# Performance work log

Hardware: AMD Instinct MI355X
Metric: run time of the kernel (lower is better)

The kernel has to match this reference:

```python
import jax, jax.numpy as jnp
import numpy as np

B, S, HID = 1, 2048, 4096
H, HKV, DFULL, D = 32, 8, 128, 96
GROUPS = H // HKV
SCALE = DFULL ** -0.5  # scaling uses the FULL head_dim per the source
ROPE_THETA = 10000.0


def setup_inputs() -> dict:
    key = jax.random.key(0)
    ks = jax.random.split(key, 8)
    hidden_states = jax.random.normal(ks[0], (B, S, HID), jnp.float32)
    # standard HF Llama RoPE tables over the FULL head dim
    inv_freq = 1.0 / (ROPE_THETA ** (jnp.arange(0, DFULL, 2, dtype=jnp.float32) / DFULL))
    ang = jnp.arange(S, dtype=jnp.float32)[:, None] * inv_freq[None, :]  # [S, DFULL/2]
    emb = jnp.concatenate([ang, ang], axis=-1)  # [S, DFULL]
    cos = jnp.cos(emb)[None]  # [1, S, DFULL]
    sin = jnp.sin(emb)[None]
    # per-kv-head frequency indices: lo half in [0, DFULL/2), hi half = lo + DFULL/2
    half, dh = DFULL // 2, D // 2
    idx_lo = jax.random.randint(ks[1], (HKV, dh), 0, half)
    indices = jnp.concatenate([idx_lo, idx_lo + half], axis=-1).astype(jnp.int32)  # [HKV, D]
    s = 0.02
    Wq = jax.random.normal(ks[2], (H * D, HID), jnp.float32) * s
    Wk = jax.random.normal(ks[3], (HKV * D, HID), jnp.float32) * s
    Wv = jax.random.normal(ks[4], (HKV * D, HID), jnp.float32) * s
    Wo = jax.random.normal(ks[5], (HID, H * D), jnp.float32) * s
    return {"hidden_states": hidden_states, "cos": cos, "sin": sin,
            "indices": indices, "Wq": Wq, "Wk": Wk, "Wv": Wv, "Wo": Wo}


def rotate_half(x):
    x1, x2 = jnp.split(x, 2, axis=-1)
    return jnp.concatenate([-x2, x1], axis=-1)


def reference(hidden_states, cos, sin, indices, Wq, Wk, Wv, Wo):
    b, s, _ = hidden_states.shape
    # QKV projections (no bias), reshape to [B, heads, S, D]
    q = (hidden_states @ Wq.T).reshape(b, s, H, D).transpose(0, 2, 1, 3)
    k = (hidden_states @ Wk.T).reshape(b, s, HKV, D).transpose(0, 2, 1, 3)
    v = (hidden_states @ Wv.T).reshape(b, s, HKV, D).transpose(0, 2, 1, 3)
    # indexed RoPE: gather per-kv-head frequencies from the full-dim tables
    cos_h = cos[:, :, indices].transpose(0, 2, 1, 3)  # [B, HKV, S, D]
    sin_h = sin[:, :, indices].transpose(0, 2, 1, 3)
    cos_q = jnp.repeat(cos_h, GROUPS, axis=1)  # [B, H, S, D]
    sin_q = jnp.repeat(sin_h, GROUPS, axis=1)
    q = q * cos_q + rotate_half(q) * sin_q
    k = k * cos_h + rotate_half(k) * sin_h
    # GQA: repeat kv to num_attention_heads
    k = jnp.repeat(k, GROUPS, axis=1)  # [B, H, S, D]
    v = jnp.repeat(v, GROUPS, axis=1)
    scores = jnp.einsum('bhqd,bhkd->bhqk', q, k) * SCALE
    causal = jnp.tril(jnp.ones((s, s), dtype=bool))
    scores = jnp.where(causal[None, None], scores, jnp.finfo(scores.dtype).min)
    probs = jax.nn.softmax(scores, axis=-1)
    out = jnp.einsum('bhqk,bhkd->bhqd', probs, v)  # [B, H, S, D]
    out = out.transpose(0, 2, 1, 3).reshape(b, s, H * D)
    return out @ Wo.T
```

## Files before the change

### kernel.cpp

```cpp
#include <hip/hip_runtime.h>

typedef unsigned short u16;
typedef unsigned int u32;
typedef __bf16 bf16x8 __attribute__((ext_vector_type(8)));
typedef float f32x4 __attribute__((ext_vector_type(4)));

#define SCALE_Q2 0.12751743443398106f

#define GLDS16(gp, lp)                                                        \
  __builtin_amdgcn_global_load_lds(                                           \
      (const __attribute__((address_space(1))) void*)(gp),                    \
      (__attribute__((address_space(3))) void*)(lp), 16, 0, 0)

__device__ __forceinline__ u16 f2bf(float f) {
  u32 u = __builtin_bit_cast(u32, f);
  u += 0x7fffu + ((u >> 16) & 1u);
  return (u16)(u >> 16);
}
__device__ __forceinline__ float bf2f(u16 b) {
  u32 u = ((u32)b) << 16;
  return __builtin_bit_cast(float, u);
}

__global__ __launch_bounds__(256) void cvt_kernel(const float* __restrict__ src,
                                                  u16* __restrict__ dst, int n4) {
  int i = blockIdx.x * 256 + threadIdx.x;
  if (i >= n4) return;
  float4 v = ((const float4*)src)[i];
  u32 lo = (u32)f2bf(v.x) | ((u32)f2bf(v.y) << 16);
  u32 hi = (u32)f2bf(v.z) | ((u32)f2bf(v.w) << 16);
  ((uint2*)dst)[i] = make_uint2(lo, hi);
}

template <bool BF16OUT>
__global__ __launch_bounds__(256) void gemm_bt(const u16* __restrict__ A,
                                               const u16* __restrict__ B,
                                               void* __restrict__ Cout,
                                               int M, int N, int K) {
  __shared__ u16 As[128 * 64];
  __shared__ u16 Bs[128 * 64];
  const int tid = threadIdx.x;
  const int w = tid >> 6, lane = tid & 63, quad = lane >> 4, c16 = lane & 15;
  const int m0 = blockIdx.y * 128, n0 = blockIdx.x * 128;
  const int wm = (w & 1) * 64, wn = (w >> 1) * 64;
  const int srow8 = lane >> 3;
  const int scg = (lane & 7) ^ srow8;

  f32x4 acc[4][4];
#pragma unroll
  for (int i = 0; i < 4; i++)
#pragma unroll
    for (int j = 0; j < 4; j++) acc[i][j] = (f32x4){0.f, 0.f, 0.f, 0.f};

  const u16* Abase = A + (size_t)(m0 + w * 8 + srow8) * K + scg * 8;
  const u16* Bbase = B + (size_t)(n0 + w * 8 + srow8) * K + scg * 8;

  for (int k0 = 0; k0 < K; k0 += 64) {
    __syncthreads();
#pragma unroll
    for (int it = 0; it < 4; it++) {
      GLDS16(Abase + (size_t)(it * 32) * K + k0, &As[(w * 8 + it * 32) * 64]);
      GLDS16(Bbase + (size_t)(it * 32) * K + k0, &Bs[(w * 8 + it * 32) * 64]);
    }
    __syncthreads();
#pragma unroll
    for (int kk = 0; kk < 2; kk++) {
      bf16x8 af[4], bf[4];
#pragma unroll
      for (int mt = 0; mt < 4; mt++) {
        int row = wm + mt * 16 + c16;
        int col = (kk * 4 + quad) ^ (row & 7);
        af[mt] = *(const bf16x8*)(&As[row * 64 + col * 8]);
      }
#pragma unroll
      for (int nt = 0; nt < 4; nt++) {
        int row = wn + nt * 16 + c16;
        int col = (kk * 4 + quad) ^ (row & 7);
        bf[nt] = *(const bf16x8*)(&Bs[row * 64 + col * 8]);
      }
#pragma unroll
      for (int mt = 0; mt < 4; mt++)
#pragma unroll
        for (int nt = 0; nt < 4; nt++)
          acc[mt][nt] = __builtin_amdgcn_mfma_f32_16x16x32_bf16(af[mt], bf[nt], acc[mt][nt], 0, 0, 0);
    }
  }
#pragma unroll
  for (int mt = 0; mt < 4; mt++)
#pragma unroll
    for (int nt = 0; nt < 4; nt++)
#pragma unroll
      for (int r = 0; r < 4; r++) {
        int m = m0 + wm + mt * 16 + quad * 4 + r;
        int n = n0 + wn + nt * 16 + c16;
        if (BF16OUT)
          ((u16*)Cout)[(size_t)m * N + n] = f2bf(acc[mt][nt][r]);
        else
          ((float*)Cout)[(size_t)m * N + n] = acc[mt][nt][r];
      }
}

__global__ __launch_bounds__(256) void rope_kernel(const u16* __restrict__ qkv,
                                                   const float* __restrict__ cosb,
                                                   const float* __restrict__ sinb,
                                                   const int* __restrict__ idxs,
                                                   u16* __restrict__ qB,
                                                   u16* __restrict__ kB) {
  u32 i = blockIdx.x * 256u + threadIdx.x;
  const u32 NQ = 2048u * 32u * 96u;
  if (i < NQ) {
    u32 s = i / 3072u, rem = i % 3072u;
    u32 h = rem / 96u, d = rem % 96u;
    u32 hkv = h >> 2;
    u32 base = s * 4608u + h * 96u + d;
    float x = bf2f(qkv[base]);
    float pv = (d < 48u) ? -bf2f(qkv[base + 48u]) : bf2f(qkv[base - 48u]);
    int idx = idxs[hkv * 96u + d];
    float c = cosb[s * 128u + idx], sn = sinb[s * 128u + idx];
    qB[(h * 2048u + s) * 96u + d] = f2bf((x * c + pv * sn) * SCALE_Q2);
  } else {
    u32 j = i - NQ;
    u32 s = j / 768u, rem = j % 768u;
    u32 hkv = rem / 96u, d = rem % 96u;
    u32 base = s * 4608u + 3072u + hkv * 96u + d;
    float x = bf2f(qkv[base]);
    float pv = (d < 48u) ? -bf2f(qkv[base + 48u]) : bf2f(qkv[base - 48u]);
    int idx = idxs[hkv * 96u + d];
    float c = cosb[s * 128u + idx], sn = sinb[s * 128u + idx];
    kB[(hkv * 2048u + s) * 96u + d] = f2bf(x * c + pv * sn);
  }
}

__global__ __launch_bounds__(256) void vtrans_kernel(const u16* __restrict__ qkvB,
                                                     u16* __restrict__ vtB) {
  __shared__ u16 T[64 * 34];
  const int s0 = blockIdx.x * 64, d0 = blockIdx.y * 32;
  const int tx = threadIdx.x & 31, ty = threadIdx.x >> 5;
#pragma unroll
  for (int it = 0; it < 8; it++) {
    int row = it * 8 + ty;
    T[row * 34 + tx] = qkvB[(size_t)(s0 + row) * 4608 + 3840 + d0 + tx];
  }
  __syncthreads();
  const int sx = threadIdx.x & 63, dy = threadIdx.x >> 6;
#pragma unroll
  for (int it = 0; it < 8; it++) {
    int d = it * 4 + dy;
    vtB[(size_t)(d0 + d) * 2048 + s0 + sx] = T[sx * 34 + d];
  }
}

__global__ __launch_bounds__(256) void attn_kernel(const u16* __restrict__ qB,
                                                   const u16* __restrict__ kB,
                                                   const u16* __restrict__ vtB,
                                                   u16* __restrict__ aoB) {
  __shared__ u16 Ks[64 * 96];
  __shared__ u16 Vs[96 * 64];
  __shared__ u16 Ps[4 * 16 * 64];
  const int tid = threadIdx.x;
  const int w = tid >> 6, lane = tid & 63, quad = lane >> 4, c16 = lane & 15;
  const int pr = blockIdx.x, h = blockIdx.y, hkv = h >> 2;
  u16* pw = Ps + w * (16 * 64);

  size_t voff[3];
#pragma unroll
  for (int it = 0; it < 3; it++) {
    int j = it * 256 + tid;
    int row = j >> 3, c = (j & 7) ^ (row & 7);
    voff[it] = (size_t)row * 2048 + c * 8;
  }
  const u16* kbase = kB + (size_t)hkv * 2048 * 96;
  const u16* vbase = vtB + (size_t)hkv * 96 * 2048;

  bf16x8 vones;
#pragma unroll
  for (int i = 0; i < 8; i++) vones[i] = (__bf16)1.0f;

  for (int ph = 0; ph < 2; ph++) {
    const int qt = ph ? (31 - pr) : pr;
    const int m_base = qt * 64 + w * 16;

    bf16x8 qf[3];
    {
      const u16* qrow = qB + ((size_t)h * 2048 + m_base + c16) * 96;
#pragma unroll
      for (int t = 0; t < 3; t++) qf[t] = *(const bf16x8*)(qrow + t * 32 + quad * 8);
    }
    f32x4 o[6], ol;
#pragma unroll
    for (int dt = 0; dt < 6; dt++) o[dt] = (f32x4){0.f, 0.f, 0.f, 0.f};
    ol = (f32x4){0.f, 0.f, 0.f, 0.f};

    for (int kt = 0; kt <= qt; kt++) {
      const int k0 = kt * 64;
      __syncthreads();
#pragma unroll
      for (int it = 0; it < 3; it++) {
        GLDS16(kbase + (size_t)k0 * 96 + (it * 256 + tid) * 8,
               &Ks[(it * 256 + w * 64) * 8]);
        GLDS16(vbase + voff[it] + k0, &Vs[(it * 256 + w * 64) * 8]);
      }
      __syncthreads();

      f32x4 sacc[4];
#pragma unroll
      for (int nt = 0; nt < 4; nt++) sacc[nt] = (f32x4){0.f, 0.f, 0.f, 0.f};
#pragma unroll
      for (int nt = 0; nt < 4; nt++)
#pragma unroll
        for (int t = 0; t < 3; t++) {
          bf16x8 kf = *(const bf16x8*)(&Ks[(nt * 16 + c16) * 96 + t * 32 + quad * 8]);
          sacc[nt] = __builtin_amdgcn_mfma_f32_16x16x32_bf16(qf[t], kf, sacc[nt], 0, 0, 0);
        }

      if (kt == qt) {
#pragma unroll
        for (int r = 0; r < 4; r++) {
          int row_abs = m_base + quad * 4 + r;
#pragma unroll
          for (int nt = 0; nt < 4; nt++)
            if (k0 + nt * 16 + c16 > row_abs) sacc[nt][r] = -__builtin_inff();
        }
      }

#pragma unroll
      for (int r = 0; r < 4; r++) {
        int mrow = quad * 4 + r, m7 = mrow & 7;
#pragma unroll
        for (int nt = 0; nt < 4; nt++) {
          float p = __builtin_amdgcn_exp2f(sacc[nt][r]);
          int chunk = (nt * 2 + (c16 >> 3)) ^ m7;
          pw[mrow * 64 + chunk * 8 + (c16 & 7)] =
              (u16)(__builtin_bit_cast(u32, p) >> 16);
        }
      }
      bf16x8 pf[2];
#pragma unroll
      for (int kti = 0; kti < 2; kti++) {
        int chunk = (kti * 4 + quad) ^ (c16 & 7);
        pf[kti] = *(const bf16x8*)(&pw[c16 * 64 + chunk * 8]);
      }
#pragma unroll
      for (int kti = 0; kti < 2; kti++) {
        ol = __builtin_amdgcn_mfma_f32_16x16x32_bf16(pf[kti], vones, ol, 0, 0, 0);
#pragma unroll
        for (int dt = 0; dt < 6; dt++) {
          int row = dt * 16 + c16;
          int vch = (kti * 4 + quad) ^ (row & 7);
          bf16x8 vf = *(const bf16x8*)(&Vs[row * 64 + vch * 8]);
          o[dt] = __builtin_amdgcn_mfma_f32_16x16x32_bf16(pf[kti], vf, o[dt], 0, 0, 0);
        }
      }
    }

#pragma unroll
    for (int r = 0; r < 4; r++) {
      float inv = 1.0f / ol[r];
      int row = m_base + quad * 4 + r;
#pragma unroll
      for (int dt = 0; dt < 6; dt++)
        aoB[(size_t)row * 3072 + h * 96 + dt * 16 + c16] = f2bf(o[dt][r] * inv);
    }
  }
}

extern "C" void kernel_launch(void* const* d_in, const int* in_sizes, int n_in,
                              void* d_out, int out_size, void* d_ws, size_t ws_size,
                              hipStream_t stream) {
  const float* hs   = (const float*)d_in[0];
  const float* cosb = (const float*)d_in[1];
  const float* sinb = (const float*)d_in[2];
  const int*   idxs = (const int*)d_in[3];
  const float* Wq   = (const float*)d_in[4];
  const float* Wk   = (const float*)d_in[5];
  const float* Wv   = (const float*)d_in[6];
  const float* Wo   = (const float*)d_in[7];
  float* out = (float*)d_out;
  char* ws = (char*)d_ws;

  u16* hsB   = (u16*)(ws);
  u16* wqkvB = (u16*)(ws + 16777216);
  u16* woB   = (u16*)(ws + 54525952);
  u16* qkvB  = (u16*)(ws + 79691776);
  u16* qB    = (u16*)(ws + 98566144);
  u16* kB    = (u16*)(ws + 111149056);
  u16* vtB   = (u16*)(ws + 114294784);
  u16* aoB   = (u16*)(ws + 117440512);

  cvt_kernel<<<8192, 256, 0, stream>>>(hs, hsB, 2097152);
  cvt_kernel<<<12288, 256, 0, stream>>>(Wq, wqkvB, 3145728);
  cvt_kernel<<<3072, 256, 0, stream>>>(Wk, wqkvB + 3072 * 4096, 786432);
  cvt_kernel<<<3072, 256, 0, stream>>>(Wv, wqkvB + 3840 * 4096, 786432);
  cvt_kernel<<<12288, 256, 0, stream>>>(Wo, woB, 3145728);

  gemm_bt<true><<<dim3(36, 16), 256, 0, stream>>>(hsB, wqkvB, qkvB, 2048, 4608, 4096);

  rope_kernel<<<30720, 256, 0, stream>>>(qkvB, cosb, sinb, idxs, qB, kB);
  vtrans_kernel<<<dim3(32, 24), 256, 0, stream>>>(qkvB, vtB);

  attn_kernel<<<dim3(16, 32), 256, 0, stream>>>(qB, kB, vtB, aoB);

  gemm_bt<false><<<dim3(32, 16), 256, 0, stream>>>(aoB, woB, out, 2048, 4096, 3072);
}
```

Measured before the change: 442.3 us.

## Replace GEMM with double-buffered 8-wave 256-row tiles and XCD-aware block remap

Replaces the single-buffered 128x128 GEMM with a 512-thread kernel that computes 256xBN tiles and double-buffers LDS. The next K-tile is prefetched with global_load_lds while the current one feeds the MFMAs, using manual vmcnt waits, s_setprio around the MFMA bursts, and a block-ID remap that groups neighbouring tiles per XCD. The aim is to hide global-load latency and raise per-tile data reuse for both the QKV and output projections. In exchange it uses more LDS and registers, and relies on hand-written waitcnt counts that must match the number of loads in flight.

```diff
diff --git a/kernel.cpp b/kernel.cpp
--- a/kernel.cpp
+++ b/kernel.cpp
@@ -32,65 +32,107 @@
   ((uint2*)dst)[i] = make_uint2(lo, hi);
 }
 
-template <bool BF16OUT>
-__global__ __launch_bounds__(256) void gemm_bt(const u16* __restrict__ A,
-                                               const u16* __restrict__ B,
-                                               void* __restrict__ Cout,
-                                               int M, int N, int K) {
-  __shared__ u16 As[128 * 64];
-  __shared__ u16 Bs[128 * 64];
+template <int NREP, bool BF16OUT>
+__global__ __launch_bounds__(512, 2) void gemm8p(const u16* __restrict__ A,
+                                                 const u16* __restrict__ B,
+                                                 void* __restrict__ Cout,
+                                                 int M, int N, int K) {
+  constexpr int BN = NREP * 64;
+  __shared__ u16 As[2 * 256 * 64];
+  __shared__ u16 Bs[2 * BN * 64];
   const int tid = threadIdx.x;
   const int w = tid >> 6, lane = tid & 63, quad = lane >> 4, c16 = lane & 15;
-  const int m0 = blockIdx.y * 128, n0 = blockIdx.x * 128;
-  const int wm = (w & 1) * 64, wn = (w >> 1) * 64;
-  const int srow8 = lane >> 3;
-  const int scg = (lane & 7) ^ srow8;
-
-  f32x4 acc[4][4];
-#pragma unroll
-  for (int i = 0; i < 4; i++)
-#pragma unroll
-    for (int j = 0; j < 4; j++) acc[i][j] = (f32x4){0.f, 0.f, 0.f, 0.f};
-
-  const u16* Abase = A + (size_t)(m0 + w * 8 + srow8) * K + scg * 8;
-  const u16* Bbase = B + (size_t)(n0 + w * 8 + srow8) * K + scg * 8;
-
-  for (int k0 = 0; k0 < K; k0 += 64) {
-    __syncthreads();
-#pragma unroll
-    for (int it = 0; it < 4; it++) {
-      GLDS16(Abase + (size_t)(it * 32) * K + k0, &As[(w * 8 + it * 32) * 64]);
-      GLDS16(Bbase + (size_t)(it * 32) * K + k0, &Bs[(w * 8 + it * 32) * 64]);
-    }
-    __syncthreads();
-#pragma unroll
-    for (int kk = 0; kk < 2; kk++) {
-      bf16x8 af[4], bf[4];
-#pragma unroll
-      for (int mt = 0; mt < 4; mt++) {
-        int row = wm + mt * 16 + c16;
-        int col = (kk * 4 + quad) ^ (row & 7);
-        af[mt] = *(const bf16x8*)(&As[row * 64 + col * 8]);
-      }
-#pragma unroll
-      for (int nt = 0; nt < 4; nt++) {
-        int row = wn + nt * 16 + c16;
-        int col = (kk * 4 + quad) ^ (row & 7);
-        bf[nt] = *(const bf16x8*)(&Bs[row * 64 + col * 8]);
-      }
-#pragma unroll
-      for (int mt = 0; mt < 4; mt++)
-#pragma unroll
-        for (int nt = 0; nt < 4; nt++)
-          acc[mt][nt] = __builtin_amdgcn_mfma_f32_16x16x32_bf16(af[mt], bf[nt], acc[mt][nt], 0, 0, 0);
-    }
-  }
-#pragma unroll
-  for (int mt = 0; mt < 4; mt++)
-#pragma unroll
-    for (int nt = 0; nt < 4; nt++)
-#pragma unroll
-      for (int r = 0; r < 4; r++) {
+
+  const int nx = gridDim.x;
+  const int orig = blockIdx.y * nx + blockIdx.x;
+  const int nwg = nx * gridDim.y;
+  const int id = (orig & 7) * (nwg >> 3) + (orig >> 3);
+  const int n0 = (id % nx) * BN, m0 = (id / nx) * 256;
+
+  const int wm = (w & 1) * 128, wn = (w >> 1) * (NREP * 16);
+  const int srow8 = lane >> 3, scg = (lane & 7) ^ srow8;
+  const u16* Ag = A + (size_t)(m0 + w * 8 + srow8) * K + scg * 8;
+  const u16* Bg = B + (size_t)(n0 + w * 8 + srow8) * K + scg * 8;
+  const int axor = c16 & 7;
+
+  f32x4 acc[8][NREP];
+#pragma unroll
+  for (int i = 0; i < 8; ++i)
+#pragma unroll
+    for (int j = 0; j < NREP; ++j) acc[i][j] = (f32x4){0.f, 0.f, 0.f, 0.f};
+
+  const int NT = K >> 6;
+
+#pragma unroll
+  for (int j = 0; j < 4; ++j)
+    GLDS16(Ag + (size_t)(j * 64) * K, &As[(j * 64 + w * 8) * 64]);
+#pragma unroll
+  for (int j = 0; j < NREP; ++j)
+    GLDS16(Bg + (size_t)(j * 64) * K, &Bs[(j * 64 + w * 8) * 64]);
+
+  for (int t = 0; t < NT; ++t) {
+    const int sl = t & 1;
+    const u16* as = &As[sl * (256 * 64)];
+    const u16* bs = &Bs[sl * (BN * 64)];
+    u16* asn = &As[(sl ^ 1) * (256 * 64)];
+    u16* bsn = &Bs[(sl ^ 1) * (BN * 64)];
+    const int kn = (t + 1) * 64;
+    const bool pf = (t + 1 < NT);
+
+    if (pf) {
+#pragma unroll
+      for (int j = 0; j < 4; ++j)
+        GLDS16(Ag + (size_t)(j * 64) * K + kn, &asn[(j * 64 + w * 8) * 64]);
+      asm volatile("s_waitcnt vmcnt(4)" ::: "memory");
+    } else {
+      asm volatile("s_waitcnt vmcnt(0)" ::: "memory");
+    }
+    __builtin_amdgcn_s_barrier();
+    asm volatile("" ::: "memory");
+
+    bf16x8 bfr[NREP][2];
+#pragma unroll
+    for (int nt = 0; nt < NREP; ++nt)
+#pragma unroll
+      for (int kk = 0; kk < 2; ++kk)
+        bfr[nt][kk] = *(const bf16x8*)&bs[(wn + nt * 16 + c16) * 64 +
+                                          (((kk * 4 + quad) ^ axor) * 8)];
+
+#pragma unroll
+    for (int ph = 0; ph < 4; ++ph) {
+      bf16x8 afr[2][2];
+#pragma unroll
+      for (int i = 0; i < 2; ++i)
+#pragma unroll
+        for (int kk = 0; kk < 2; ++kk)
+          afr[i][kk] = *(const bf16x8*)&as[(wm + (ph * 2 + i) * 16 + c16) * 64 +
+                                            (((kk * 4 + quad) ^ axor) * 8)];
+      if (ph == 1 && pf) {
+#pragma unroll
+        for (int j = 0; j < NREP; ++j)
+          GLDS16(Bg + (size_t)(j * 64) * K + kn, &bsn[(j * 64 + w * 8) * 64]);
+      }
+      __builtin_amdgcn_s_setprio(1);
+#pragma unroll
+      for (int i = 0; i < 2; ++i)
+#pragma unroll
+        for (int nt = 0; nt < NREP; ++nt)
+#pragma unroll
+          for (int kk = 0; kk < 2; ++kk)
+            acc[ph * 2 + i][nt] = __builtin_amdgcn_mfma_f32_16x16x32_bf16(
+                afr[i][kk], bfr[nt][kk], acc[ph * 2 + i][nt], 0, 0, 0);
+      __builtin_amdgcn_s_setprio(0);
+    }
+    asm volatile("" ::: "memory");
+    __builtin_amdgcn_s_barrier();
+  }
+
+#pragma unroll
+  for (int mt = 0; mt < 8; ++mt)
+#pragma unroll
+    for (int nt = 0; nt < NREP; ++nt)
+#pragma unroll
+      for (int r = 0; r < 4; ++r) {
         int m = m0 + wm + mt * 16 + quad * 4 + r;
         int n = n0 + wn + nt * 16 + c16;
         if (BF16OUT)
@@ -293,12 +335,12 @@
   cvt_kernel<<<3072, 256, 0, stream>>>(Wv, wqkvB + 3840 * 4096, 786432);
   cvt_kernel<<<12288, 256, 0, stream>>>(Wo, woB, 3145728);
 
-  gemm_bt<true><<<dim3(36, 16), 256, 0, stream>>>(hsB, wqkvB, qkvB, 2048, 4608, 4096);
+  gemm8p<3, true><<<dim3(24, 8), 512, 0, stream>>>(hsB, wqkvB, qkvB, 2048, 4608, 4096);
 
   rope_kernel<<<30720, 256, 0, stream>>>(qkvB, cosb, sinb, idxs, qB, kB);
   vtrans_kernel<<<dim3(32, 24), 256, 0, stream>>>(qkvB, vtB);
 
   attn_kernel<<<dim3(16, 32), 256, 0, stream>>>(qB, kB, vtB, aoB);
 
-  gemm_bt<false><<<dim3(32, 16), 256, 0, stream>>>(aoB, woB, out, 2048, 4096, 3072);
-}
+  gemm8p<2, false><<<dim3(32, 8), 512, 0, stream>>>(aoB, woB, out, 2048, 4096, 3072);
+}
```

Measured after the change: 439.5 us. No clear change (-0.6%).
